# Kernel optimization log

Measured on AMD Instinct MI355X. Metric: run time of the kernel, lower is better.

Reference implementation:

```python
import jax, jax.numpy as jnp
import numpy as np

B, N, E, HQ, HKV = 4, 8192, 1024, 16, 16
EPS = 1e-5


def act_quant(x):
    # per-token absmax 8-bit fake quant (BitNet b1.58 activation quant)
    scale = 127.0 / jnp.clip(jnp.max(jnp.abs(x), axis=-1, keepdims=True), 1e-5, None)
    return jnp.clip(jnp.round(x * scale), -128, 127) / scale


def weight_quant(w):
    # absmean ternary {-1,0,1} fake quant
    scale = 1.0 / jnp.clip(jnp.mean(jnp.abs(w)), 1e-5, None)
    return jnp.clip(jnp.round(w * scale), -1, 1) / scale


def bitlinear(x, w, b):
    # straight-through estimator: quantized forward, identity backward
    xq = x + jax.lax.stop_gradient(act_quant(x) - x)
    wq = w + jax.lax.stop_gradient(weight_quant(w) - w)
    return jnp.einsum('bne,oe->bno', xq, wq) + b


def setup_inputs() -> dict:
    k0 = jax.random.key(0)
    ks = jax.random.split(k0, 8)
    kv_e = E // HQ * HKV
    xavier = lambda k, o, i: jax.random.normal(k, (o, i), jnp.float32) * np.sqrt(2.0 / (o + i))
    return {
        'query': jax.random.normal(ks[0], (B, N, E), jnp.float32),
        'key': jax.random.normal(ks[1], (B, N, E), jnp.float32),
        'value': jax.random.normal(ks[2], (B, N, E), jnp.float32),
        'Wq': xavier(ks[3], E, E), 'bq': jnp.zeros((E,), jnp.float32),
        'Wk': xavier(ks[4], kv_e, E), 'bk': jnp.zeros((kv_e,), jnp.float32),
        'Wv': xavier(ks[5], kv_e, E), 'bv': jnp.zeros((kv_e,), jnp.float32),
        'gamma': jnp.ones((kv_e,), jnp.float32), 'beta': jnp.zeros((kv_e,), jnp.float32),
        'Wo': xavier(ks[6], E, kv_e), 'bo': jnp.zeros((E,), jnp.float32),
    }


def reference(query, key, value, Wq, bq, Wk, bk, Wv, bv, gamma, beta, Wo, bo):
    q = bitlinear(query, Wq, bq).reshape(B, N, HQ, -1)   # [B,N,HQ,d]
    k = bitlinear(key, Wk, bk).reshape(B, N, HKV, -1)    # [B,N,HKV,d]
    v = bitlinear(value, Wv, bv).reshape(B, N, HKV, -1)
    d = q.shape[-1]
    scale = d ** 0.5
    # faithful to source: layout is 'b n h d', so attention mixes over HEADS per token
    sim = jnp.einsum('bnhd,bngd->bnhg', q / scale, k)    # [B,N,HQ,HKV]
    attn = jax.nn.softmax(sim, axis=-1)
    x = jnp.einsum('bnhg,bngd->bnhd', attn, v).reshape(B, N, HQ * d)
    mu = jnp.mean(x, axis=-1, keepdims=True)
    var = jnp.var(x, axis=-1, keepdims=True)
    x = (x - mu) * jax.lax.rsqrt(var + EPS) * gamma + beta
    return bitlinear(x, Wo, bo)
```

## Files before the change

kernel.cpp:

```cpp
#include <hip/hip_runtime.h>
#include <stdint.h>

#define NTOK 32768
#define NE   1024
#define NWEL 1048576

typedef int v4i __attribute__((ext_vector_type(4)));
typedef __attribute__((ext_vector_type(8))) short bhalf8;
typedef __attribute__((ext_vector_type(4))) float f32x4;

__device__ __forceinline__ float wave_sum(float v) {
#pragma unroll
  for (int o = 32; o; o >>= 1) v += __shfl_xor(v, o, 64);
  return v;
}
__device__ __forceinline__ float wave_max(float v) {
#pragma unroll
  for (int o = 32; o; o >>= 1) v = fmaxf(v, __shfl_xor(v, o, 64));
  return v;
}

__device__ __forceinline__ void gload_lds16(const void* gptr, void* ldsptr) {
  __builtin_amdgcn_global_load_lds(
      (const __attribute__((address_space(1))) void*)gptr,
      (__attribute__((address_space(3))) void*)ldsptr, 16, 0, 0);
}

__device__ __forceinline__ unsigned bf_rne(float f) {
  unsigned u = __float_as_uint(f);
  return (u + 0x7fffu + ((u >> 16) & 1u)) >> 16;
}
__device__ __forceinline__ float bf_f(unsigned h) { return __uint_as_float(h << 16); }

__device__ __forceinline__ void split8(const float* e, bhalf8& hi, bhalf8& lo) {
  union { int i[4]; bhalf8 v; } H, L;
#pragma unroll
  for (int w = 0; w < 4; ++w) {
    unsigned h0 = bf_rne(e[2 * w]), h1 = bf_rne(e[2 * w + 1]);
    unsigned l0 = bf_rne(e[2 * w] - bf_f(h0));
    unsigned l1 = bf_rne(e[2 * w + 1] - bf_f(h1));
    H.i[w] = (int)(h0 | (h1 << 16));
    L.i[w] = (int)(l0 | (l1 << 16));
  }
  hi = H.v; lo = L.v;
}

__global__ __launch_bounds__(256) void wabs_kernel(
    const float* __restrict__ Wq, const float* __restrict__ Wk,
    const float* __restrict__ Wv, const float* __restrict__ Wo,
    float* __restrict__ part) {
  const int widx = blockIdx.y;
  const float* W = widx == 0 ? Wq : widx == 1 ? Wk : widx == 2 ? Wv : Wo;
  const float4* W4 = (const float4*)W;
  const int tid = threadIdx.x;
  size_t base = (size_t)blockIdx.x * 256 + tid;
  float s = 0.f;
#pragma unroll
  for (int i = 0; i < 4; ++i) {
    float4 w = W4[base + (size_t)i * 65536];
    s += fabsf(w.x) + fabsf(w.y) + fabsf(w.z) + fabsf(w.w);
  }
  s = wave_sum(s);
  __shared__ float red[4];
  if ((tid & 63) == 0) red[tid >> 6] = s;
  __syncthreads();
  if (tid == 0) part[widx * 256 + blockIdx.x] = red[0] + red[1] + red[2] + red[3];
}

__global__ __launch_bounds__(256) void wmean_kernel(
    const float* __restrict__ part, float* __restrict__ wmean) {
  const int b = blockIdx.x;
  float v = part[b * 256 + threadIdx.x];
  v = wave_sum(v);
  __shared__ float red[4];
  if ((threadIdx.x & 63) == 0) red[threadIdx.x >> 6] = v;
  __syncthreads();
  if (threadIdx.x == 0)
    wmean[b] = fmaxf((red[0] + red[1] + red[2] + red[3]) * (1.0f / 1048576.0f), 1e-5f);
}

__global__ __launch_bounds__(256) void wquant_kernel(
    const float* __restrict__ Wq, const float* __restrict__ Wk,
    const float* __restrict__ Wv, const float* __restrict__ Wo,
    signed char* __restrict__ out, const float* __restrict__ wmean) {
  const int widx = blockIdx.y;
  const float* W = widx == 0 ? Wq : widx == 1 ? Wk : widx == 2 ? Wv : Wo;
  const float scale = 1.0f / wmean[widx];
  size_t i4 = (size_t)blockIdx.x * 256 + threadIdx.x;
  float4 w = ((const float4*)W)[i4];
  char4 q;
  q.x = (signed char)fminf(fmaxf(rintf(w.x * scale), -1.f), 1.f);
  q.y = (signed char)fminf(fmaxf(rintf(w.y * scale), -1.f), 1.f);
  q.z = (signed char)fminf(fmaxf(rintf(w.z * scale), -1.f), 1.f);
  q.w = (signed char)fminf(fmaxf(rintf(w.w * scale), -1.f), 1.f);
  ((char4*)(out + (size_t)widx * NWEL))[i4] = q;
}

__global__ __launch_bounds__(256) void actquant_kernel(
    const float* __restrict__ in0, const float* __restrict__ in1, const float* __restrict__ in2,
    signed char* __restrict__ o0, signed char* __restrict__ o1, signed char* __restrict__ o2,
    float* __restrict__ r0, float* __restrict__ r1, float* __restrict__ r2) {
  const int which = blockIdx.y;
  const float* x = which == 0 ? in0 : which == 1 ? in1 : in2;
  signed char* xq = which == 0 ? o0 : which == 1 ? o1 : o2;
  float* rs = which == 0 ? r0 : which == 1 ? r1 : r2;
  const int row = blockIdx.x, tid = threadIdx.x;
  float4 v = ((const float4*)(x + (size_t)row * NE))[tid];
  float am = fmaxf(fmaxf(fabsf(v.x), fabsf(v.y)), fmaxf(fabsf(v.z), fabsf(v.w)));
  am = wave_max(am);
  __shared__ float red[4];
  if ((tid & 63) == 0) red[tid >> 6] = am;
  __syncthreads();
  am = fmaxf(fmaxf(red[0], red[1]), fmaxf(red[2], red[3]));
  float cm = fmaxf(am, 1e-5f);
  float scale = 127.0f / cm;
  char4 q;
  q.x = (signed char)fminf(fmaxf(rintf(v.x * scale), -128.f), 127.f);
  q.y = (signed char)fminf(fmaxf(rintf(v.y * scale), -128.f), 127.f);
  q.z = (signed char)fminf(fmaxf(rintf(v.z * scale), -128.f), 127.f);
  q.w = (signed char)fminf(fmaxf(rintf(v.w * scale), -128.f), 127.f);
  ((char4*)(xq + (size_t)row * NE))[tid] = q;
  if (tid == 0) rs[row] = cm * (1.0f / 127.0f);
}

__global__ __launch_bounds__(256) void gemm_kernel(
    const signed char* __restrict__ A, const signed char* __restrict__ B,
    const float* __restrict__ rowscale, const float* __restrict__ wmeanp,
    const float* __restrict__ bias, float* __restrict__ C) {
  __shared__ signed char As[128 * 64];
  __shared__ signed char Bs[128 * 64];
  const int tid = threadIdx.x;
  const int lane = tid & 63, wid = tid >> 6;
  const int wr = wid >> 1, wc = wid & 1;
  const int bm = blockIdx.y, bn = blockIdx.x;
  const signed char* Ab = A + (size_t)bm * 128 * 1024;
  const signed char* Bb = B + (size_t)bn * 128 * 1024;

  v4i acc[4][4];
#pragma unroll
  for (int i = 0; i < 4; ++i)
#pragma unroll
    for (int j = 0; j < 4; ++j) acc[i][j] = (v4i){0, 0, 0, 0};

  const int o0 = wid * 2048 + lane * 16;
  const int r0 = o0 >> 6, c0 = o0 & 63;
  const int o1 = o0 + 1024;
  const int r1 = o1 >> 6, c1 = o1 & 63;
  const int klo = (lane >> 4) << 4;
  const int arow0 = (wr * 64 + (lane & 15)) * 64 + klo;
  const int brow0 = (wc * 64 + (lane & 15)) * 64 + klo;

  for (int k0 = 0; k0 < 1024; k0 += 64) {
    gload_lds16(Ab + (size_t)r0 * 1024 + k0 + c0, &As[wid * 2048]);
    gload_lds16(Ab + (size_t)r1 * 1024 + k0 + c1, &As[wid * 2048 + 1024]);
    gload_lds16(Bb + (size_t)r0 * 1024 + k0 + c0, &Bs[wid * 2048]);
    gload_lds16(Bb + (size_t)r1 * 1024 + k0 + c1, &Bs[wid * 2048 + 1024]);
    __syncthreads();
    v4i af[4], bf[4];
#pragma unroll
    for (int i = 0; i < 4; ++i) af[i] = *(const v4i*)&As[arow0 + i * 16 * 64];
#pragma unroll
    for (int j = 0; j < 4; ++j) bf[j] = *(const v4i*)&Bs[brow0 + j * 16 * 64];
#pragma unroll
    for (int i = 0; i < 4; ++i)
#pragma unroll
      for (int j = 0; j < 4; ++j)
        acc[i][j] = __builtin_amdgcn_mfma_i32_16x16x64_i8(af[i], bf[j], acc[i][j], 0, 0, 0);
    __syncthreads();
  }

  const float wmean = *wmeanp;
  const int row0 = bm * 128 + wr * 64 + ((lane >> 4) << 2);
  const int col0 = bn * 128 + wc * 64 + (lane & 15);
#pragma unroll
  for (int i = 0; i < 4; ++i) {
#pragma unroll
    for (int r = 0; r < 4; ++r) {
      const int m = row0 + i * 16 + r;
      const float rsw = rowscale[m] * wmean;
#pragma unroll
      for (int j = 0; j < 4; ++j) {
        const int n = col0 + j * 16;
        C[(size_t)m * 1024 + n] = (float)acc[i][j][r] * rsw + bias[n];
      }
    }
  }
}

__global__ __launch_bounds__(256) void attn_kernel(
    const float* __restrict__ qf, const float* __restrict__ kf,
    const float* __restrict__ vf, const float* __restrict__ gamma,
    const float* __restrict__ beta, signed char* __restrict__ xq,
    float* __restrict__ rs) {
  __shared__ unsigned p32s[4][16 * 20];
  const int tid = threadIdx.x;
  const int lane = tid & 63, wid = tid >> 6;
  const int token = blockIdx.x * 4 + wid;
  const float* qrow = qf + (size_t)token * 1024;
  const float* krow = kf + (size_t)token * 1024;
  const float* vrow = vf + (size_t)token * 1024;

  const int fr = lane & 15;
  const int fg = lane >> 4;
  const int g0 = (fg & 1) * 8;

  float qe0[8], qe1[8], ke0[8], ke1[8];
  {
    float4 a0 = *(const float4*)(qrow + fr * 64 + fg * 8);
    float4 a1 = *(const float4*)(qrow + fr * 64 + fg * 8 + 4);
    float4 a2 = *(const float4*)(qrow + fr * 64 + 32 + fg * 8);
    float4 a3 = *(const float4*)(qrow + fr * 64 + 32 + fg * 8 + 4);
    qe0[0]=a0.x; qe0[1]=a0.y; qe0[2]=a0.z; qe0[3]=a0.w;
    qe0[4]=a1.x; qe0[5]=a1.y; qe0[6]=a1.z; qe0[7]=a1.w;
    qe1[0]=a2.x; qe1[1]=a2.y; qe1[2]=a2.z; qe1[3]=a2.w;
    qe1[4]=a3.x; qe1[5]=a3.y; qe1[6]=a3.z; qe1[7]=a3.w;
    float4 b0 = *(const float4*)(krow + fr * 64 + fg * 8);
    float4 b1 = *(const float4*)(krow + fr * 64 + fg * 8 + 4);
    float4 b2 = *(const float4*)(krow + fr * 64 + 32 + fg * 8);
    float4 b3 = *(const float4*)(krow + fr * 64 + 32 + fg * 8 + 4);
    ke0[0]=b0.x; ke0[1]=b0.y; ke0[2]=b0.z; ke0[3]=b0.w;
    ke0[4]=b1.x; ke0[5]=b1.y; ke0[6]=b1.z; ke0[7]=b1.w;
    ke1[0]=b2.x; ke1[1]=b2.y; ke1[2]=b2.z; ke1[3]=b2.w;
    ke1[4]=b3.x; ke1[5]=b3.y; ke1[6]=b3.z; ke1[7]=b3.w;
  }
  float val[4][8];
#pragma unroll
  for (int j = 0; j < 4; ++j)
#pragma unroll
    for (int i = 0; i < 8; ++i)
      val[j][i] = vrow[(g0 + i) * 64 + 16 * j + fr];

  bhalf8 qh0, ql0, qh1, ql1, kh0, kl0, kh1, kl1;
  split8(qe0, qh0, ql0); split8(qe1, qh1, ql1);
  split8(ke0, kh0, kl0); split8(ke1, kh1, kl1);
  f32x4 sacc = {0.f, 0.f, 0.f, 0.f};
  sacc = __builtin_amdgcn_mfma_f32_16x16x32_bf16(qh0, kh0, sacc, 0, 0, 0);
  sacc = __builtin_amdgcn_mfma_f32_16x16x32_bf16(qh0, kl0, sacc, 0, 0, 0);
  sacc = __builtin_amdgcn_mfma_f32_16x16x32_bf16(ql0, kh0, sacc, 0, 0, 0);
  sacc = __builtin_amdgcn_mfma_f32_16x16x32_bf16(qh1, kh1, sacc, 0, 0, 0);
  sacc = __builtin_amdgcn_mfma_f32_16x16x32_bf16(qh1, kl1, sacc, 0, 0, 0);
  sacc = __builtin_amdgcn_mfma_f32_16x16x32_bf16(ql1, kh1, sacc, 0, 0, 0);

  float p[4];
#pragma unroll
  for (int r = 0; r < 4; ++r) {
    float s = sacc[r] * 0.125f;
    float mx = s;
#pragma unroll
    for (int o = 8; o; o >>= 1) mx = fmaxf(mx, __shfl_xor(mx, o, 16));
    float e = __expf(s - mx);
    float sum = e;
#pragma unroll
    for (int o = 8; o; o >>= 1) sum += __shfl_xor(sum, o, 16);
    p[r] = e / sum;
  }

  unsigned* ps = p32s[wid];
#pragma unroll
  for (int r = 0; r < 4; ++r) {
    unsigned h16 = bf_rne(p[r]);
    unsigned l16 = bf_rne(p[r] - bf_f(h16));
    ps[(fg * 4 + r) * 20 + fr] = h16 | (l16 << 16);
  }
  int4 pa = *(const int4*)&ps[fr * 20 + g0];
  int4 pb = *(const int4*)&ps[fr * 20 + g0 + 4];
  bhalf8 A1, A2;
  {
    const unsigned sh = (fg >= 2) ? 16u : 0u;
    union { int i[4]; bhalf8 v; } U, Z;
    U.i[0] = (int)(((pa.x >> sh) & 0xffffu) | (((pa.y >> sh) & 0xffffu) << 16));
    U.i[1] = (int)(((pa.z >> sh) & 0xffffu) | (((pa.w >> sh) & 0xffffu) << 16));
    U.i[2] = (int)(((pb.x >> sh) & 0xffffu) | (((pb.y >> sh) & 0xffffu) << 16));
    U.i[3] = (int)(((pb.z >> sh) & 0xffffu) | (((pb.w >> sh) & 0xffffu) << 16));
    A1 = U.v;
    Z.i[0] = (fg >= 2) ? 0 : U.i[0];
    Z.i[1] = (fg >= 2) ? 0 : U.i[1];
    Z.i[2] = (fg >= 2) ? 0 : U.i[2];
    Z.i[3] = (fg >= 2) ? 0 : U.i[3];
    A2 = Z.v;
  }

  f32x4 pacc[4];
#pragma unroll
  for (int j = 0; j < 4; ++j) {
    bhalf8 Bh, Bl;
    split8(val[j], Bh, Bl);
    f32x4 a = {0.f, 0.f, 0.f, 0.f};
    a = __builtin_amdgcn_mfma_f32_16x16x32_bf16(A1, Bh, a, 0, 0, 0);
    a = __builtin_amdgcn_mfma_f32_16x16x32_bf16(A2, Bl, a, 0, 0, 0);
    pacc[j] = a;
  }

  float s = 0.f, sq = 0.f;
#pragma unroll
  for (int j = 0; j < 4; ++j)
#pragma unroll
    for (int r = 0; r < 4; ++r) {
      float x = pacc[j][r];
      s += x; sq += x * x;
    }
  s = wave_sum(s); sq = wave_sum(sq);
  const float mu = s * (1.0f / 1024.0f);
  const float var = sq * (1.0f / 1024.0f) - mu * mu;
  const float rstd = rsqrtf(var + 1e-5f);

  float y[16];
  float am = 0.f;
#pragma unroll
  for (int j = 0; j < 4; ++j)
#pragma unroll
    for (int r = 0; r < 4; ++r) {
      const int idx = (fg * 4 + r) * 64 + 16 * j + fr;
      float yy = (pacc[j][r] - mu) * rstd * gamma[idx] + beta[idx];
      y[j * 4 + r] = yy;
      am = fmaxf(am, fabsf(yy));
    }
  am = wave_max(am);
  const float cm = fmaxf(am, 1e-5f);
  const float scale = 127.0f / cm;
  signed char* orow = xq + (size_t)token * 1024;
#pragma unroll
  for (int j = 0; j < 4; ++j)
#pragma unroll
    for (int r = 0; r < 4; ++r) {
      const int idx = (fg * 4 + r) * 64 + 16 * j + fr;
      orow[idx] = (signed char)fminf(fmaxf(rintf(y[j * 4 + r] * scale), -128.f), 127.f);
    }
  if (lane == 0) rs[token] = cm * (1.0f / 127.0f);
}

extern "C" void kernel_launch(void* const* d_in, const int* in_sizes, int n_in,
                              void* d_out, int out_size, void* d_ws, size_t ws_size,
                              hipStream_t stream) {
  const float* query = (const float*)d_in[0];
  const float* key   = (const float*)d_in[1];
  const float* value = (const float*)d_in[2];
  const float* Wq = (const float*)d_in[3];
  const float* bq = (const float*)d_in[4];
  const float* Wk = (const float*)d_in[5];
  const float* bk = (const float*)d_in[6];
  const float* Wv = (const float*)d_in[7];
  const float* bv = (const float*)d_in[8];
  const float* gamma = (const float*)d_in[9];
  const float* beta  = (const float*)d_in[10];
  const float* Wo = (const float*)d_in[11];
  const float* bo = (const float*)d_in[12];

  uint8_t* ws = (uint8_t*)d_ws;
  signed char* wqt = (signed char*)ws;
  float* wpart = (float*)(ws + ((size_t)4 << 20));
  float* wmean = (float*)(ws + ((size_t)4 << 20) + 16384);
  float* rs_q = (float*)(ws + ((size_t)5 << 20));
  float* rs_k = rs_q + NTOK;
  float* rs_v = rs_k + NTOK;
  float* rs_a = rs_v + NTOK;
  signed char* xq_q = (signed char*)(ws + ((size_t)8 << 20));
  signed char* xq_k = xq_q + ((size_t)32 << 20);
  signed char* xq_v = xq_k + ((size_t)32 << 20);
  signed char* xq_a = xq_q;
  float* qf = (float*)(ws + ((size_t)104 << 20));
  float* kf = (float*)(ws + ((size_t)232 << 20));
  float* vf = (float*)d_out;
  float* out = (float*)d_out;

  wabs_kernel<<<dim3(256, 4), 256, 0, stream>>>(Wq, Wk, Wv, Wo, wpart);
  wmean_kernel<<<4, 256, 0, stream>>>(wpart, wmean);
  wquant_kernel<<<dim3(1024, 4), 256, 0, stream>>>(Wq, Wk, Wv, Wo, wqt, wmean);
  actquant_kernel<<<dim3(NTOK, 3), 256, 0, stream>>>(query, key, value,
                                                     xq_q, xq_k, xq_v, rs_q, rs_k, rs_v);
  gemm_kernel<<<dim3(8, 256), 256, 0, stream>>>(xq_q, wqt + 0 * (size_t)NWEL, rs_q, wmean + 0, bq, qf);
  gemm_kernel<<<dim3(8, 256), 256, 0, stream>>>(xq_k, wqt + 1 * (size_t)NWEL, rs_k, wmean + 1, bk, kf);
  gemm_kernel<<<dim3(8, 256), 256, 0, stream>>>(xq_v, wqt + 2 * (size_t)NWEL, rs_v, wmean + 2, bv, vf);
  attn_kernel<<<NTOK / 4, 256, 0, stream>>>(qf, kf, vf, gamma, beta, xq_a, rs_a);
  gemm_kernel<<<dim3(8, 256), 256, 0, stream>>>(xq_a, wqt + 3 * (size_t)NWEL, rs_a, wmean + 3, bo, out);
}
```

Before: 802.5 us.

## Double-buffer GEMM with 128-wide K tiles, swizzled LDS, and per-wave actquant rows

The int8 GEMM now stages 128-wide K tiles into two LDS buffers, prefetching the next tile while MFMAs run on the current one. An XOR swizzle on the LDS column is meant to avoid bank conflicts on fragment reads. The activation-quant kernel now gives each wave one row, which removes the LDS reduction and the block barrier. LDS use per block rises to 64KB, which may lower occupancy.

New measurement: 803.4 us. Within noise of the previous version (+0.1%).

```diff
diff --git a/kernel.cpp b/kernel.cpp
--- a/kernel.cpp
+++ b/kernel.cpp
@@ -104,31 +104,61 @@
   const float* x = which == 0 ? in0 : which == 1 ? in1 : in2;
   signed char* xq = which == 0 ? o0 : which == 1 ? o1 : o2;
   float* rs = which == 0 ? r0 : which == 1 ? r1 : r2;
-  const int row = blockIdx.x, tid = threadIdx.x;
-  float4 v = ((const float4*)(x + (size_t)row * NE))[tid];
-  float am = fmaxf(fmaxf(fabsf(v.x), fabsf(v.y)), fmaxf(fabsf(v.z), fabsf(v.w)));
+  const int tid = threadIdx.x, lane = tid & 63, wid = tid >> 6;
+  const int row = blockIdx.x * 4 + wid;
+  const float4* r4 = (const float4*)(x + (size_t)row * NE);
+  float4 v0 = r4[lane], v1 = r4[64 + lane], v2 = r4[128 + lane], v3 = r4[192 + lane];
+  float am = 0.f;
+  am = fmaxf(am, fmaxf(fmaxf(fabsf(v0.x), fabsf(v0.y)), fmaxf(fabsf(v0.z), fabsf(v0.w))));
+  am = fmaxf(am, fmaxf(fmaxf(fabsf(v1.x), fabsf(v1.y)), fmaxf(fabsf(v1.z), fabsf(v1.w))));
+  am = fmaxf(am, fmaxf(fmaxf(fabsf(v2.x), fabsf(v2.y)), fmaxf(fabsf(v2.z), fabsf(v2.w))));
+  am = fmaxf(am, fmaxf(fmaxf(fabsf(v3.x), fabsf(v3.y)), fmaxf(fabsf(v3.z), fabsf(v3.w))));
   am = wave_max(am);
-  __shared__ float red[4];
-  if ((tid & 63) == 0) red[tid >> 6] = am;
-  __syncthreads();
-  am = fmaxf(fmaxf(red[0], red[1]), fmaxf(red[2], red[3]));
-  float cm = fmaxf(am, 1e-5f);
-  float scale = 127.0f / cm;
+  const float cm = fmaxf(am, 1e-5f);
+  const float scale = 127.0f / cm;
   char4 q;
-  q.x = (signed char)fminf(fmaxf(rintf(v.x * scale), -128.f), 127.f);
-  q.y = (signed char)fminf(fmaxf(rintf(v.y * scale), -128.f), 127.f);
-  q.z = (signed char)fminf(fmaxf(rintf(v.z * scale), -128.f), 127.f);
-  q.w = (signed char)fminf(fmaxf(rintf(v.w * scale), -128.f), 127.f);
-  ((char4*)(xq + (size_t)row * NE))[tid] = q;
-  if (tid == 0) rs[row] = cm * (1.0f / 127.0f);
+  char4* o4 = (char4*)(xq + (size_t)row * NE);
+  q.x = (signed char)fminf(fmaxf(rintf(v0.x * scale), -128.f), 127.f);
+  q.y = (signed char)fminf(fmaxf(rintf(v0.y * scale), -128.f), 127.f);
+  q.z = (signed char)fminf(fmaxf(rintf(v0.z * scale), -128.f), 127.f);
+  q.w = (signed char)fminf(fmaxf(rintf(v0.w * scale), -128.f), 127.f);
+  o4[lane] = q;
+  q.x = (signed char)fminf(fmaxf(rintf(v1.x * scale), -128.f), 127.f);
+  q.y = (signed char)fminf(fmaxf(rintf(v1.y * scale), -128.f), 127.f);
+  q.z = (signed char)fminf(fmaxf(rintf(v1.z * scale), -128.f), 127.f);
+  q.w = (signed char)fminf(fmaxf(rintf(v1.w * scale), -128.f), 127.f);
+  o4[64 + lane] = q;
+  q.x = (signed char)fminf(fmaxf(rintf(v2.x * scale), -128.f), 127.f);
+  q.y = (signed char)fminf(fmaxf(rintf(v2.y * scale), -128.f), 127.f);
+  q.z = (signed char)fminf(fmaxf(rintf(v2.z * scale), -128.f), 127.f);
+  q.w = (signed char)fminf(fmaxf(rintf(v2.w * scale), -128.f), 127.f);
+  o4[128 + lane] = q;
+  q.x = (signed char)fminf(fmaxf(rintf(v3.x * scale), -128.f), 127.f);
+  q.y = (signed char)fminf(fmaxf(rintf(v3.y * scale), -128.f), 127.f);
+  q.z = (signed char)fminf(fmaxf(rintf(v3.z * scale), -128.f), 127.f);
+  q.w = (signed char)fminf(fmaxf(rintf(v3.w * scale), -128.f), 127.f);
+  o4[192 + lane] = q;
+  if (lane == 0) rs[row] = cm * (1.0f / 127.0f);
+}
+
+__device__ __forceinline__ void stage_tile(const signed char* __restrict__ Gb,
+                                           signed char* lds_base, int k0,
+                                           int wid, int lane) {
+  const int rbase = wid * 32 + (lane >> 3);
+  const int col = ((lane & 7) ^ (lane >> 3)) << 4;
+#pragma unroll
+  for (int c = 0; c < 4; ++c) {
+    gload_lds16(Gb + (size_t)(rbase + c * 8) * 1024 + k0 + col,
+                lds_base + wid * 4096 + c * 1024);
+  }
 }
 
 __global__ __launch_bounds__(256) void gemm_kernel(
     const signed char* __restrict__ A, const signed char* __restrict__ B,
     const float* __restrict__ rowscale, const float* __restrict__ wmeanp,
     const float* __restrict__ bias, float* __restrict__ C) {
-  __shared__ signed char As[128 * 64];
-  __shared__ signed char Bs[128 * 64];
+  __shared__ signed char As[2][16384];
+  __shared__ signed char Bs[2][16384];
   const int tid = threadIdx.x;
   const int lane = tid & 63, wid = tid >> 6;
   const int wr = wid >> 1, wc = wid & 1;
@@ -142,31 +172,49 @@
 #pragma unroll
     for (int j = 0; j < 4; ++j) acc[i][j] = (v4i){0, 0, 0, 0};
 
-  const int o0 = wid * 2048 + lane * 16;
-  const int r0 = o0 >> 6, c0 = o0 & 63;
-  const int o1 = o0 + 1024;
-  const int r1 = o1 >> 6, c1 = o1 & 63;
-  const int klo = (lane >> 4) << 4;
-  const int arow0 = (wr * 64 + (lane & 15)) * 64 + klo;
-  const int brow0 = (wc * 64 + (lane & 15)) * 64 + klo;
-
-  for (int k0 = 0; k0 < 1024; k0 += 64) {
-    gload_lds16(Ab + (size_t)r0 * 1024 + k0 + c0, &As[wid * 2048]);
-    gload_lds16(Ab + (size_t)r1 * 1024 + k0 + c1, &As[wid * 2048 + 1024]);
-    gload_lds16(Bb + (size_t)r0 * 1024 + k0 + c0, &Bs[wid * 2048]);
-    gload_lds16(Bb + (size_t)r1 * 1024 + k0 + c1, &Bs[wid * 2048 + 1024]);
+  const int fr15 = lane & 15;
+  const int kq = (lane >> 4) << 4;
+
+  stage_tile(Ab, As[0], 0, wid, lane);
+  stage_tile(Bb, Bs[0], 0, wid, lane);
+  __syncthreads();
+
+  int cur = 0;
+  for (int t = 0; t < 8; ++t) {
+    if (t < 7) {
+      stage_tile(Ab, As[cur ^ 1], (t + 1) * 128, wid, lane);
+      stage_tile(Bb, Bs[cur ^ 1], (t + 1) * 128, wid, lane);
+    }
+    v4i af[4][2], bf[4][2];
+#pragma unroll
+    for (int i = 0; i < 4; ++i) {
+      const int r = wr * 64 + i * 16 + fr15;
+      const int sw = (r & 7) << 4;
+#pragma unroll
+      for (int kk = 0; kk < 2; ++kk) {
+        const int ko = kk * 64 + kq;
+        af[i][kk] = *(const v4i*)&As[cur][r * 128 + (ko ^ sw)];
+      }
+    }
+#pragma unroll
+    for (int j = 0; j < 4; ++j) {
+      const int r = wc * 64 + j * 16 + fr15;
+      const int sw = (r & 7) << 4;
+#pragma unroll
+      for (int kk = 0; kk < 2; ++kk) {
+        const int ko = kk * 64 + kq;
+        bf[j][kk] = *(const v4i*)&Bs[cur][r * 128 + (ko ^ sw)];
+      }
+    }
+#pragma unroll
+    for (int i = 0; i < 4; ++i)
+#pragma unroll
+      for (int j = 0; j < 4; ++j) {
+        acc[i][j] = __builtin_amdgcn_mfma_i32_16x16x64_i8(af[i][0], bf[j][0], acc[i][j], 0, 0, 0);
+        acc[i][j] = __builtin_amdgcn_mfma_i32_16x16x64_i8(af[i][1], bf[j][1], acc[i][j], 0, 0, 0);
+      }
     __syncthreads();
-    v4i af[4], bf[4];
-#pragma unroll
-    for (int i = 0; i < 4; ++i) af[i] = *(const v4i*)&As[arow0 + i * 16 * 64];
-#pragma unroll
-    for (int j = 0; j < 4; ++j) bf[j] = *(const v4i*)&Bs[brow0 + j * 16 * 64];
-#pragma unroll
-    for (int i = 0; i < 4; ++i)
-#pragma unroll
-      for (int j = 0; j < 4; ++j)
-        acc[i][j] = __builtin_amdgcn_mfma_i32_16x16x64_i8(af[i], bf[j], acc[i][j], 0, 0, 0);
-    __syncthreads();
+    cur ^= 1;
   }
 
   const float wmean = *wmeanp;
@@ -366,8 +414,8 @@
   wabs_kernel<<<dim3(256, 4), 256, 0, stream>>>(Wq, Wk, Wv, Wo, wpart);
   wmean_kernel<<<4, 256, 0, stream>>>(wpart, wmean);
   wquant_kernel<<<dim3(1024, 4), 256, 0, stream>>>(Wq, Wk, Wv, Wo, wqt, wmean);
-  actquant_kernel<<<dim3(NTOK, 3), 256, 0, stream>>>(query, key, value,
-                                                     xq_q, xq_k, xq_v, rs_q, rs_k, rs_v);
+  actquant_kernel<<<dim3(NTOK / 4, 3), 256, 0, stream>>>(query, key, value,
+                                                         xq_q, xq_k, xq_v, rs_q, rs_k, rs_v);
   gemm_kernel<<<dim3(8, 256), 256, 0, stream>>>(xq_q, wqt + 0 * (size_t)NWEL, rs_q, wmean + 0, bq, qf);
   gemm_kernel<<<dim3(8, 256), 256, 0, stream>>>(xq_k, wqt + 1 * (size_t)NWEL, rs_k, wmean + 1, bk, kf);
   gemm_kernel<<<dim3(8, 256), 256, 0, stream>>>(xq_v, wqt + 2 * (size_t)NWEL, rs_v, wmean + 2, bv, vf);
```

## Pipeline int8 GEMM with 4-stage LDS ring, XOR swizzle, and wave-per-row act quant

Applied to the files above, without the earlier changes.

The int8 GEMM now uses a 4-deep LDS ring buffer, prefetching three k-tiles ahead. Each iteration waits with explicit vmcnt counts and a single barrier, so global-to-LDS loads overlap MFMA work. LDS columns are XOR-swizzled by row to reduce bank conflicts on fragment reads. The activation quant kernel now handles two rows per wave and eight rows per block, using only wave shuffles with no shared-memory reduction or block sync, which cuts launch count. The cost is four times the LDS use per block, which may lower occupancy, plus fragile hand-counted waitcnt logic.

Measured after the change: 853.2 us. 1.06x slower.

```diff
diff --git a/kernel.cpp b/kernel.cpp
--- a/kernel.cpp
+++ b/kernel.cpp
@@ -96,6 +96,18 @@
   ((char4*)(out + (size_t)widx * NWEL))[i4] = q;
 }
 
+__device__ __forceinline__ char4 quant4(float4 v, float scale) {
+  char4 q;
+  q.x = (signed char)fminf(fmaxf(rintf(v.x * scale), -128.f), 127.f);
+  q.y = (signed char)fminf(fmaxf(rintf(v.y * scale), -128.f), 127.f);
+  q.z = (signed char)fminf(fmaxf(rintf(v.z * scale), -128.f), 127.f);
+  q.w = (signed char)fminf(fmaxf(rintf(v.w * scale), -128.f), 127.f);
+  return q;
+}
+__device__ __forceinline__ float amax4(float4 v) {
+  return fmaxf(fmaxf(fabsf(v.x), fabsf(v.y)), fmaxf(fabsf(v.z), fabsf(v.w)));
+}
+
 __global__ __launch_bounds__(256) void actquant_kernel(
     const float* __restrict__ in0, const float* __restrict__ in1, const float* __restrict__ in2,
     signed char* __restrict__ o0, signed char* __restrict__ o1, signed char* __restrict__ o2,
@@ -104,31 +116,48 @@
   const float* x = which == 0 ? in0 : which == 1 ? in1 : in2;
   signed char* xq = which == 0 ? o0 : which == 1 ? o1 : o2;
   float* rs = which == 0 ? r0 : which == 1 ? r1 : r2;
-  const int row = blockIdx.x, tid = threadIdx.x;
-  float4 v = ((const float4*)(x + (size_t)row * NE))[tid];
-  float am = fmaxf(fmaxf(fabsf(v.x), fabsf(v.y)), fmaxf(fabsf(v.z), fabsf(v.w)));
-  am = wave_max(am);
-  __shared__ float red[4];
-  if ((tid & 63) == 0) red[tid >> 6] = am;
-  __syncthreads();
-  am = fmaxf(fmaxf(red[0], red[1]), fmaxf(red[2], red[3]));
-  float cm = fmaxf(am, 1e-5f);
-  float scale = 127.0f / cm;
-  char4 q;
-  q.x = (signed char)fminf(fmaxf(rintf(v.x * scale), -128.f), 127.f);
-  q.y = (signed char)fminf(fmaxf(rintf(v.y * scale), -128.f), 127.f);
-  q.z = (signed char)fminf(fmaxf(rintf(v.z * scale), -128.f), 127.f);
-  q.w = (signed char)fminf(fmaxf(rintf(v.w * scale), -128.f), 127.f);
-  ((char4*)(xq + (size_t)row * NE))[tid] = q;
-  if (tid == 0) rs[row] = cm * (1.0f / 127.0f);
+  const int tid = threadIdx.x, lane = tid & 63, wid = tid >> 6;
+  const int row = blockIdx.x * 8 + wid * 2;
+  const float4* ra = (const float4*)(x + (size_t)row * NE);
+  const float4* rb = (const float4*)(x + (size_t)(row + 1) * NE);
+  float4 a0 = ra[lane], a1 = ra[64 + lane], a2 = ra[128 + lane], a3 = ra[192 + lane];
+  float4 b0 = rb[lane], b1 = rb[64 + lane], b2 = rb[128 + lane], b3 = rb[192 + lane];
+  float ama = fmaxf(fmaxf(amax4(a0), amax4(a1)), fmaxf(amax4(a2), amax4(a3)));
+  float amb = fmaxf(fmaxf(amax4(b0), amax4(b1)), fmaxf(amax4(b2), amax4(b3)));
+#pragma unroll
+  for (int o = 32; o; o >>= 1) {
+    ama = fmaxf(ama, __shfl_xor(ama, o, 64));
+    amb = fmaxf(amb, __shfl_xor(amb, o, 64));
+  }
+  const float cma = fmaxf(ama, 1e-5f), cmb = fmaxf(amb, 1e-5f);
+  const float sa = 127.0f / cma, sb = 127.0f / cmb;
+  char4* oa = (char4*)(xq + (size_t)row * NE);
+  char4* ob = (char4*)(xq + (size_t)(row + 1) * NE);
+  oa[lane] = quant4(a0, sa); oa[64 + lane] = quant4(a1, sa);
+  oa[128 + lane] = quant4(a2, sa); oa[192 + lane] = quant4(a3, sa);
+  ob[lane] = quant4(b0, sb); ob[64 + lane] = quant4(b1, sb);
+  ob[128 + lane] = quant4(b2, sb); ob[192 + lane] = quant4(b3, sb);
+  if (lane == 0) { rs[row] = cma * (1.0f / 127.0f); rs[row + 1] = cmb * (1.0f / 127.0f); }
+}
+
+__device__ __forceinline__ void stage_mat(const signed char* __restrict__ Gb,
+                                          signed char* lds_buf, int k0,
+                                          int wid, int lane) {
+  const int r0 = wid * 32 + (lane >> 2);
+  const int col = ((lane & 3) ^ ((lane >> 2) & 3)) << 4;
+#pragma unroll
+  for (int q = 0; q < 2; ++q) {
+    gload_lds16(Gb + (size_t)(r0 + q * 16) * 1024 + k0 + col,
+                lds_buf + wid * 2048 + q * 1024);
+  }
 }
 
 __global__ __launch_bounds__(256) void gemm_kernel(
     const signed char* __restrict__ A, const signed char* __restrict__ B,
     const float* __restrict__ rowscale, const float* __restrict__ wmeanp,
     const float* __restrict__ bias, float* __restrict__ C) {
-  __shared__ signed char As[128 * 64];
-  __shared__ signed char Bs[128 * 64];
+  __shared__ signed char As[4][8192];
+  __shared__ signed char Bs[4][8192];
   const int tid = threadIdx.x;
   const int lane = tid & 63, wid = tid >> 6;
   const int wr = wid >> 1, wc = wid & 1;
@@ -142,36 +171,48 @@
 #pragma unroll
     for (int j = 0; j < 4; ++j) acc[i][j] = (v4i){0, 0, 0, 0};
 
-  const int o0 = wid * 2048 + lane * 16;
-  const int r0 = o0 >> 6, c0 = o0 & 63;
-  const int o1 = o0 + 1024;
-  const int r1 = o1 >> 6, c1 = o1 & 63;
-  const int klo = (lane >> 4) << 4;
-  const int arow0 = (wr * 64 + (lane & 15)) * 64 + klo;
-  const int brow0 = (wc * 64 + (lane & 15)) * 64 + klo;
-
-  for (int k0 = 0; k0 < 1024; k0 += 64) {
-    gload_lds16(Ab + (size_t)r0 * 1024 + k0 + c0, &As[wid * 2048]);
-    gload_lds16(Ab + (size_t)r1 * 1024 + k0 + c1, &As[wid * 2048 + 1024]);
-    gload_lds16(Bb + (size_t)r0 * 1024 + k0 + c0, &Bs[wid * 2048]);
-    gload_lds16(Bb + (size_t)r1 * 1024 + k0 + c1, &Bs[wid * 2048 + 1024]);
-    __syncthreads();
+  const int fr15 = lane & 15;
+  const int kq = (lane >> 4) << 4;
+
+  stage_mat(Ab, As[0], 0, wid, lane);
+  stage_mat(Bb, Bs[0], 0, wid, lane);
+  stage_mat(Ab, As[1], 64, wid, lane);
+  stage_mat(Bb, Bs[1], 64, wid, lane);
+  stage_mat(Ab, As[2], 128, wid, lane);
+  stage_mat(Bb, Bs[2], 128, wid, lane);
+
+  for (int kt = 0; kt < 16; ++kt) {
+    const int s = kt & 3;
+    if (kt < 14)      asm volatile("s_waitcnt vmcnt(8)" ::: "memory");
+    else if (kt == 14) asm volatile("s_waitcnt vmcnt(4)" ::: "memory");
+    else               asm volatile("s_waitcnt vmcnt(0)" ::: "memory");
+    __builtin_amdgcn_s_barrier();
+    __builtin_amdgcn_sched_barrier(0);
+    if (kt < 13) {
+      stage_mat(Ab, As[(kt + 3) & 3], (kt + 3) * 64, wid, lane);
+      stage_mat(Bb, Bs[(kt + 3) & 3], (kt + 3) * 64, wid, lane);
+    }
     v4i af[4], bf[4];
 #pragma unroll
-    for (int i = 0; i < 4; ++i) af[i] = *(const v4i*)&As[arow0 + i * 16 * 64];
-#pragma unroll
-    for (int j = 0; j < 4; ++j) bf[j] = *(const v4i*)&Bs[brow0 + j * 16 * 64];
+    for (int i = 0; i < 4; ++i) {
+      const int r = wr * 64 + i * 16 + fr15;
+      af[i] = *(const v4i*)&As[s][r * 64 + (kq ^ ((r & 3) << 4))];
+    }
+#pragma unroll
+    for (int j = 0; j < 4; ++j) {
+      const int r = wc * 64 + j * 16 + fr15;
+      bf[j] = *(const v4i*)&Bs[s][r * 64 + (kq ^ ((r & 3) << 4))];
+    }
 #pragma unroll
     for (int i = 0; i < 4; ++i)
 #pragma unroll
       for (int j = 0; j < 4; ++j)
         acc[i][j] = __builtin_amdgcn_mfma_i32_16x16x64_i8(af[i], bf[j], acc[i][j], 0, 0, 0);
-    __syncthreads();
   }
 
   const float wmean = *wmeanp;
   const int row0 = bm * 128 + wr * 64 + ((lane >> 4) << 2);
-  const int col0 = bn * 128 + wc * 64 + (lane & 15);
+  const int col0 = bn * 128 + wc * 64 + fr15;
 #pragma unroll
   for (int i = 0; i < 4; ++i) {
 #pragma unroll
@@ -366,8 +407,8 @@
   wabs_kernel<<<dim3(256, 4), 256, 0, stream>>>(Wq, Wk, Wv, Wo, wpart);
   wmean_kernel<<<4, 256, 0, stream>>>(wpart, wmean);
   wquant_kernel<<<dim3(1024, 4), 256, 0, stream>>>(Wq, Wk, Wv, Wo, wqt, wmean);
-  actquant_kernel<<<dim3(NTOK, 3), 256, 0, stream>>>(query, key, value,
-                                                     xq_q, xq_k, xq_v, rs_q, rs_k, rs_v);
+  actquant_kernel<<<dim3(NTOK / 8, 3), 256, 0, stream>>>(query, key, value,
+                                                         xq_q, xq_k, xq_v, rs_q, rs_k, rs_v);
   gemm_kernel<<<dim3(8, 256), 256, 0, stream>>>(xq_q, wqt + 0 * (size_t)NWEL, rs_q, wmean + 0, bq, qf);
   gemm_kernel<<<dim3(8, 256), 256, 0, stream>>>(xq_k, wqt + 1 * (size_t)NWEL, rs_k, wmean + 1, bk, kf);
   gemm_kernel<<<dim3(8, 256), 256, 0, stream>>>(xq_v, wqt + 2 * (size_t)NWEL, rs_v, wmean + 2, bv, vf);
```
